# Optimization experiments

Measured on AMD Instinct MI355X. Metric: run time of the kernel, lower is better.

Reference implementation:

```python
import jax, jax.numpy as jnp
import numpy as np

NUM_HEADS = 12


def _quantize_feat(feat, embed):
    # feat: [B,H,M,d], embed: [H,K,d] -> nearest codebook vector per token
    # squared euclidean distance (same argmin as cdist p=2)
    f2 = jnp.sum(feat * feat, axis=-1, keepdims=True)            # [B,H,M,1]
    e2 = jnp.sum(embed * embed, axis=-1)[None, :, None, :]       # [1,H,1,K]
    fe = jnp.einsum('bhmd,hkd->bhmk', feat, embed)               # [B,H,M,K]
    dist = f2 - 2.0 * fe + e2
    idx = jnp.argmin(dist, axis=-1)                              # [B,H,M]
    quant = jnp.take_along_axis(embed[None], idx[..., None], axis=2)  # [B,H,M,d]
    return quant


def setup_inputs() -> dict:
    key = jax.random.key(0)
    ks = jax.random.split(key, 6)
    B, N, C, H, K = 64, 197, 768, NUM_HEADS, 50
    d = C // H
    return {
        'x': jax.random.normal(ks[0], (B, N, C), jnp.float32),
        'qkv_w': jax.random.normal(ks[1], (3 * C, C), jnp.float32) * (C ** -0.5),
        'proj_w': jax.random.normal(ks[2], (C, C), jnp.float32) * (C ** -0.5),
        'proj_b': jnp.zeros((C,), jnp.float32),
        'q_embed': jax.random.normal(ks[3], (H, K, d), jnp.float32),
        'k_embed': jax.random.normal(ks[4], (H, K, d), jnp.float32),
    }


def reference(x, qkv_w, proj_w, proj_b, q_embed, k_embed):
    B, N, C = x.shape
    H = NUM_HEADS
    d = C // H
    scale = d ** -0.5

    qkv = jnp.einsum('bnc,oc->bno', x, qkv_w).reshape(B, N, 3, H, d)
    qkv = jnp.transpose(qkv, (2, 0, 3, 1, 4))                    # [3,B,H,N,d]
    q, k, v = qkv[0], qkv[1], qkv[2]

    attn = jax.nn.softmax(jnp.einsum('bhnd,bhmd->bhnm', q, k) * scale, axis=-1)

    # quantize all tokens except cls (index 0); cls passes through detached
    q_cls = jax.lax.stop_gradient(q[:, :, 0:1, :])
    k_cls = jax.lax.stop_gradient(k[:, :, 0:1, :])
    quant_q = _quantize_feat(q[:, :, 1:, :], q_embed)
    quant_k = _quantize_feat(k[:, :, 1:, :], k_embed)

    cat_q = jnp.concatenate((q_cls, quant_q), axis=2)
    cat_k = jnp.concatenate((k_cls, quant_k), axis=2)
    quant_attn = jax.nn.softmax(
        jnp.einsum('bhnd,bhmd->bhnm', cat_q, cat_k) * scale, axis=-1)

    # losses (matching F.mse_loss mean reduction and F.kl_div semantics,
    # where input is treated as log-probabilities)
    q_tgt = jax.lax.stop_gradient(q[:, :, 1:, :])
    k_tgt = jax.lax.stop_gradient(k[:, :, 1:, :])
    quant_loss = jnp.mean((quant_q - q_tgt) ** 2) + jnp.mean((quant_k - k_tgt) ** 2)
    attn_det = jax.lax.stop_gradient(attn)
    kl = jnp.mean(attn_det * (jnp.log(attn_det) - quant_attn))
    quant_loss = quant_loss + kl

    out = jnp.einsum('bhnm,bhmd->bhnd', quant_attn, v)           # [B,H,N,d]
    out = jnp.transpose(out, (0, 2, 1, 3)).reshape(B, N, C)
    out = jnp.einsum('bnc,oc->bno', out, proj_w) + proj_b
    return (out, quant_loss)
```

## Files before the change

kernel.cpp:

```cpp
#include <hip/hip_runtime.h>
#include <math.h>

#define NB 64
#define NN 197
#define NC 768
#define NH 12
#define ND 64
#define KCB 50
#define NM (NN-1)
#define BNROWS (NB*NN)
#define SZ ((size_t)NB*NH*NN*ND)
#define WQKV ((size_t)2304*768)
#define WPRJ ((size_t)768*768)

typedef unsigned short u16;
typedef unsigned int u32;
typedef unsigned long long u64;
typedef _Float16 h2 __attribute__((ext_vector_type(2)));
typedef _Float16 f16x4 __attribute__((ext_vector_type(4)));
typedef _Float16 f16x8 __attribute__((ext_vector_type(8)));
typedef float f32x4 __attribute__((ext_vector_type(4)));

#define GLOAD16(gp, lp) __builtin_amdgcn_global_load_lds( \
    (const __attribute__((address_space(1))) void*)(gp),  \
    (__attribute__((address_space(3))) void*)(lp), 16, 0, 0)

__device__ __forceinline__ u16 f2h(float x) {
  _Float16 h = (_Float16)x;
  return *(u16*)&h;
}
__device__ __forceinline__ float h2f(u16 b) { _Float16 h = *(_Float16*)&b; return (float)h; }

#define XQ4 ((int)(SZ/4))
#define WQ4 ((int)(WQKV/4))
#define PQ4 ((int)(WPRJ/4))
#define TOTQ4 (XQ4 + WQ4 + PQ4)

__global__ __launch_bounds__(256)
void split_all(const float* __restrict__ x, const float* __restrict__ qkv_w,
               const float* __restrict__ proj_w,
               u16* __restrict__ xh, u16* __restrict__ xl,
               u16* __restrict__ wh, u16* __restrict__ wl,
               u16* __restrict__ ph)
{
  for (int i = blockIdx.x*256 + threadIdx.x; i < TOTQ4; i += gridDim.x*256) {
    const float* src; u16* hi; u16* lo; int j;
    if (i < XQ4)            { src = x;      hi = xh; lo = xl;      j = i; }
    else if (i < XQ4+WQ4)   { src = qkv_w;  hi = wh; lo = wl;      j = i - XQ4; }
    else                    { src = proj_w; hi = ph; lo = nullptr; j = i - XQ4 - WQ4; }
    float4 v = ((const float4*)src)[j];
    _Float16 h0 = (_Float16)v.x, h1 = (_Float16)v.y, h2_ = (_Float16)v.z, h3 = (_Float16)v.w;
    uint2 hv = make_uint2((u32)*(u16*)&h0 | ((u32)*(u16*)&h1 << 16),
                          (u32)*(u16*)&h2_ | ((u32)*(u16*)&h3 << 16));
    ((uint2*)hi)[j] = hv;
    if (lo) {
      _Float16 l0 = (_Float16)(v.x - (float)h0), l1 = (_Float16)(v.y - (float)h1);
      _Float16 l2 = (_Float16)(v.z - (float)h2_), l3 = (_Float16)(v.w - (float)h3);
      uint2 lv = make_uint2((u32)*(u16*)&l0 | ((u32)*(u16*)&l1 << 16),
                            (u32)*(u16*)&l2 | ((u32)*(u16*)&l3 << 16));
      ((uint2*)lo)[j] = lv;
    }
  }
}

template<int MODE>
__global__ __launch_bounds__(256)
void gemm_mfma(const u16* __restrict__ Ah, const u16* __restrict__ Al,
               const u16* __restrict__ Wh, const u16* __restrict__ Wl,
               u16* __restrict__ qh_, u16* __restrict__ ql_,
               u16* __restrict__ kh_, u16* __restrict__ kl_, u16* __restrict__ vb_,
               const float* __restrict__ bias, float* __restrict__ dout)
{
  constexpr int NPL = (MODE == 1) ? 2 : 4;
  constexpr int NBX = (MODE == 1) ? 6 : 18;
  constexpr int NWG = NBX * 99;
  constexpr int Q8 = NWG / 8, R8 = NWG % 8;
  __shared__ u16 lds[2][NPL][4096];
  const int tid = threadIdx.x;
  const int lane = tid & 63, w = tid >> 6;
  const int wm = w >> 1, wn = w & 1;
  const int wg = blockIdx.x;
  const int xcd = wg & 7, cidx = wg >> 3;
  const int work = (xcd < R8 ? xcd*(Q8+1) : R8*(Q8+1) + (xcd-R8)*Q8) + cidx;
  const int row0 = (work / NBX) * 128, col0 = (work % NBX) * 128;
  const bool dolo = (MODE == 0) && (col0 < 1536);

  f32x4 acc[4][4];
  #pragma unroll
  for (int mi = 0; mi < 4; ++mi)
    #pragma unroll
    for (int ni = 0; ni < 4; ++ni) acc[mi][ni] = (f32x4){0.f, 0.f, 0.f, 0.f};

  auto stage = [&](int buf, int kt) {
    const int c0 = kt * 32;
    #pragma unroll
    for (int j = 0; j < 2; ++j) {
      const int r0 = w*32 + j*16;
      const int lrow = r0 + (lane >> 2);
      const int slot = (lane & 3) ^ (lrow & 3);
      int ar = row0 + lrow; if (ar > BNROWS-1) ar = BNROWS-1;
      const size_t ga = (size_t)ar * 768 + c0 + slot*8;
      const size_t gb = (size_t)(col0 + lrow) * 768 + c0 + slot*8;
      GLOAD16(Ah + ga, &lds[buf][0][r0*32]);
      GLOAD16(Wh + gb, &lds[buf][1][r0*32]);
      if constexpr (MODE == 0) {
        if (dolo) {
          GLOAD16(Al + ga, &lds[buf][2][r0*32]);
          GLOAD16(Wl + gb, &lds[buf][3][r0*32]);
        }
      }
    }
  };

  auto compute = [&](int buf) {
    f16x8 ah[4], bh[4];
    const int g = lane >> 4;
    int offa[4], offb[4];
    #pragma unroll
    for (int mi = 0; mi < 4; ++mi) {
      int arow = wm*64 + mi*16 + (lane & 15);
      offa[mi] = arow*32 + ((g ^ (arow & 3)) << 3);
      ah[mi] = *(const f16x8*)&lds[buf][0][offa[mi]];
    }
    #pragma unroll
    for (int ni = 0; ni < 4; ++ni) {
      int brow = wn*64 + ni*16 + (lane & 15);
      offb[ni] = brow*32 + ((g ^ (brow & 3)) << 3);
      bh[ni] = *(const f16x8*)&lds[buf][1][offb[ni]];
    }
    #pragma unroll
    for (int mi = 0; mi < 4; ++mi)
      #pragma unroll
      for (int ni = 0; ni < 4; ++ni)
        acc[mi][ni] = __builtin_amdgcn_mfma_f32_16x16x32_f16(ah[mi], bh[ni], acc[mi][ni], 0, 0, 0);
    if constexpr (MODE == 0) {
      if (dolo) {
        f16x8 al[4], bl[4];
        #pragma unroll
        for (int mi = 0; mi < 4; ++mi) al[mi] = *(const f16x8*)&lds[buf][2][offa[mi]];
        #pragma unroll
        for (int ni = 0; ni < 4; ++ni) bl[ni] = *(const f16x8*)&lds[buf][3][offb[ni]];
        #pragma unroll
        for (int mi = 0; mi < 4; ++mi)
          #pragma unroll
          for (int ni = 0; ni < 4; ++ni) {
            acc[mi][ni] = __builtin_amdgcn_mfma_f32_16x16x32_f16(ah[mi], bl[ni], acc[mi][ni], 0, 0, 0);
            acc[mi][ni] = __builtin_amdgcn_mfma_f32_16x16x32_f16(al[mi], bh[ni], acc[mi][ni], 0, 0, 0);
          }
      }
    }
  };

  stage(0, 0);
  asm volatile("s_waitcnt vmcnt(0)" ::: "memory");
  __syncthreads();
  int cur = 0;
  for (int kt = 0; kt < 24; ++kt) {
    if (kt < 23) stage(cur ^ 1, kt + 1);
    compute(cur);
    asm volatile("s_waitcnt vmcnt(0)" ::: "memory");
    __syncthreads();
    cur ^= 1;
  }

  float* biasl = nullptr;
  if constexpr (MODE == 1) {
    biasl = (float*)&lds[0][0][0];
    if (tid < 128) biasl[tid] = bias[col0 + tid];
    __syncthreads();
  }
  #pragma unroll
  for (int mi = 0; mi < 4; ++mi) {
    #pragma unroll
    for (int t = 0; t < 4; ++t) {
      int r = row0 + wm*64 + mi*16 + (lane >> 4)*4 + t;
      if (r >= BNROWS) continue;
      if constexpr (MODE == 0) {
        int b_ = r / 197, n_ = r - b_*197;
        #pragma unroll
        for (int ni = 0; ni < 4; ++ni) {
          int o = col0 + wn*64 + ni*16 + (lane & 15);
          float val = acc[mi][ni][t];
          int tq = o / 768, rem = o - tq*768;
          int hh = rem >> 6, dd = rem & 63;
          size_t dst = ((size_t)(b_*12 + hh)*197 + n_)*64 + dd;
          u16 hi = f2h(val);
          if (tq == 0)      { qh_[dst] = hi; ql_[dst] = f2h(val - h2f(hi)); }
          else if (tq == 1) { kh_[dst] = hi; kl_[dst] = f2h(val - h2f(hi)); }
          else              vb_[dst] = hi;
        }
      } else {
        #pragma unroll
        for (int ni = 0; ni < 4; ++ni) {
          int o = col0 + wn*64 + ni*16 + (lane & 15);
          dout[(size_t)r*768 + o] = acc[mi][ni][t] + biasl[o - col0];
        }
      }
    }
  }
}

__global__ __launch_bounds__(256)
void quant_mfma(const float* __restrict__ x, const float* __restrict__ qkv_w,
                const u16* __restrict__ qh, const u16* __restrict__ ql,
                const u16* __restrict__ kh, const u16* __restrict__ kl,
                const float* __restrict__ qe, const float* __restrict__ ke,
                u16* __restrict__ cq, u16* __restrict__ ck, float* __restrict__ pq)
{
  __shared__ __align__(16) float El[KCB*66];
  __shared__ __align__(16) u16 Ehi[64*64];
  __shared__ __align__(16) u16 Elo[64*64];
  __shared__ double e2d[KCB];
  __shared__ int idxb[NM];
  __shared__ float wred[4];
  const int tid = threadIdx.x;
  const int bh = blockIdx.x;
  const int which = blockIdx.y;
  const int b_ = bh / 12, h_ = bh - b_*12;
  const u16* feath = which ? kh : qh;
  const u16* featl = which ? kl : ql;
  const float* emb  = which ? ke : qe;
  u16* dst = which ? ck : cq;
  const size_t base = (size_t)bh * (197*64);
  const int lane = tid & 63, w = tid >> 6;
  const int ln = lane & 15, g = lane >> 4;

  for (int idx = tid; idx < KCB*64; idx += 256) {
    int kk = idx >> 6, i = idx & 63;
    float v = emb[h_*(KCB*64) + idx];
    El[kk*66 + i] = v;
    _Float16 hv = (_Float16)v;
    Ehi[idx] = *(u16*)&hv;
    _Float16 lv = (_Float16)(v - (float)hv);
    Elo[idx] = *(u16*)&lv;
  }
  for (int idx = tid; idx < 14*64; idx += 256) {
    Ehi[KCB*64 + idx] = 0; Elo[KCB*64 + idx] = 0;
  }
  if (tid >= 64 && tid < 128) {
    int i = tid - 64;
    dst[base + i] = feath[base + i];
  }
  __syncthreads();
  if (tid < KCB) {
    double s = 0.0;
    for (int i = 0; i < 64; ++i) { double e = (double)El[tid*66 + i]; s += e*e; }
    e2d[tid] = s;
  }
  __syncthreads();

  f16x8 Eah[4][2], Eal[4][2];
  float e2l[4][4];
  #pragma unroll
  for (int t = 0; t < 4; ++t) {
    #pragma unroll
    for (int s = 0; s < 2; ++s) {
      int off = (t*16 + ln)*64 + s*32 + g*8;
      Eah[t][s] = *(const f16x8*)&Ehi[off];
      Eal[t][s] = *(const f16x8*)&Elo[off];
    }
    #pragma unroll
    for (int r = 0; r < 4; ++r) {
      int c = t*16 + g*4 + r;
      e2l[t][r] = (c < KCB) ? (float)e2d[c] : 1e30f;
    }
  }

  float msum = 0.f;
  for (int nt = w; nt < 13; nt += 4) {
    int tok = nt*16 + ln;
    int tokc = tok < NM ? tok : NM-1;
    const u16* fh = feath + base + (size_t)(tokc+1)*64;
    const u16* fl = featl + base + (size_t)(tokc+1)*64;
    f16x8 fqh[2], fql[2];
    float f2 = 0.f;
    #pragma unroll
    for (int s = 0; s < 2; ++s) {
      uint4 uh = *(const uint4*)(fh + s*32 + g*8);
      uint4 ul = *(const uint4*)(fl + s*32 + g*8);
      fqh[s] = *(f16x8*)&uh;
      fql[s] = *(f16x8*)&ul;
      #pragma unroll
      for (int i = 0; i < 8; ++i) {
        float q = (float)fqh[s][i] + (float)fql[s][i];
        f2 = fmaf(q, q, f2);
      }
    }
    f32x4 dacc[4];
    #pragma unroll
    for (int t = 0; t < 4; ++t) dacc[t] = (f32x4){0.f,0.f,0.f,0.f};
    #pragma unroll
    for (int t = 0; t < 4; ++t)
      #pragma unroll
      for (int s = 0; s < 2; ++s) {
        dacc[t] = __builtin_amdgcn_mfma_f32_16x16x32_f16(Eah[t][s], fqh[s], dacc[t], 0, 0, 0);
        dacc[t] = __builtin_amdgcn_mfma_f32_16x16x32_f16(Eah[t][s], fql[s], dacc[t], 0, 0, 0);
        dacc[t] = __builtin_amdgcn_mfma_f32_16x16x32_f16(Eal[t][s], fqh[s], dacc[t], 0, 0, 0);
      }
    float d1 = 1e38f, d2 = 1e38f; int idx = 0;
    #pragma unroll
    for (int t = 0; t < 4; ++t)
      #pragma unroll
      for (int r = 0; r < 4; ++r) {
        int c = t*16 + g*4 + r;
        float d = fmaf(-2.f, dacc[t][r], e2l[t][r]);
        if (d < d1) { d2 = d1; d1 = d; idx = c; }
        else if (d < d2) d2 = d;
      }
    #pragma unroll
    for (int off = 16; off <= 32; off <<= 1) {
      float od1 = __shfl_xor(d1, off), od2 = __shfl_xor(d2, off);
      int   oi  = __shfl_xor(idx, off);
      float of2 = __shfl_xor(f2, off);
      f2 += of2;
      if (od1 < d1 || (od1 == d1 && oi < idx)) {
        d2 = fminf(d1, od2); d1 = od1; idx = oi;
      } else {
        d2 = fminf(d2, od1);
      }
    }
    bool valid = tok < NM;
    bool exact = false;
    u64 flags = __ballot(g == 0 && valid && (d2 - d1) < 1e-3f);
    while (flags) {
      int src = __ffsll(flags) - 1;
      flags &= flags - 1;
      int mrow = 1 + nt*16 + src;
      const float* xrow = x + (size_t)(b_*197 + mrow)*768;
      const float* wrow = qkv_w + (size_t)(which*768 + h_*64 + lane)*768;
      double qd0 = 0.0, qd1 = 0.0, qd2 = 0.0, qd3 = 0.0;
      for (int c = 0; c < 768; c += 4) {
        qd0 = fma((double)xrow[c],   (double)wrow[c],   qd0);
        qd1 = fma((double)xrow[c+1], (double)wrow[c+1], qd1);
        qd2 = fma((double)xrow[c+2], (double)wrow[c+2], qd2);
        qd3 = fma((double)xrow[c+3], (double)wrow[c+3], qd3);
      }
      double qd = (qd0 + qd1) + (qd2 + qd3);
      double bb = 1e300; int bi = 0;
      for (int kk = 0; kk < KCB; ++kk) {
        double df = qd - (double)El[kk*66 + lane];
        double sq = df*df;
        #pragma unroll
        for (int off = 32; off > 0; off >>= 1) sq += __shfl_xor(sq, off);
        if (sq < bb) { bb = sq; bi = kk; }
      }
      if (ln == src) { idx = bi; d1 = (float)bb; exact = true; }
    }
    if (g == 0 && valid) {
      idxb[tok] = idx;
      msum += exact ? d1 : (d1 + f2);
    }
  }
  __syncthreads();

  for (int idx = tid; idx < NM*64; idx += 256) {
    int mm = idx >> 6, i = idx & 63;
    dst[base + (size_t)(mm+1)*64 + i] = f2h(El[idxb[mm]*66 + i]);
  }

  #pragma unroll
  for (int off = 8; off > 0; off >>= 1) msum += __shfl_down(msum, off);
  if (lane == 0) wred[w] = msum;
  __syncthreads();
  if (tid == 0) pq[which*768 + bh] = wred[0]+wred[1]+wred[2]+wred[3];
}

__global__ __launch_bounds__(256)
void fused_attn_mfma(const u16* __restrict__ qh, const u16* __restrict__ kh,
                     const u16* __restrict__ cq, const u16* __restrict__ ck,
                     const u16* __restrict__ vb,
                     u16* __restrict__ aoh, float* __restrict__ pkl)
{
  __shared__ __align__(16) u16 Kf[200*64];
  __shared__ __align__(16) u16 CKf[200*64];
  __shared__ __align__(16) u16 Vt[64*212];
  __shared__ float wred[4];
  const int tid = threadIdx.x;
  const int bh = blockIdx.x;
  const int b_ = bh / 12, h_ = bh - b_*12;
  const size_t base = (size_t)bh * (197*64);
  const u32* kh32 = (const u32*)kh;
  const u32* ck32 = (const u32*)ck;
  const u32* vb32 = (const u32*)vb;
  const size_t base2 = base >> 1;

  for (int idx = tid; idx < 197*32; idx += 256) {
    int m = idx >> 5, j = idx & 31;
    int dsti = m*32 + (((j >> 2) ^ (m & 7)) << 2) + (j & 3);
    ((u32*)Kf)[dsti] = kh32[base2 + idx];
    ((u32*)CKf)[dsti] = ck32[base2 + idx];
    u32 v2 = vb32[base2 + idx];
    Vt[(2*j)*212 + m]   = (u16)(v2 & 0xffff);
    Vt[(2*j+1)*212 + m] = (u16)(v2 >> 16);
  }
  for (int idx = tid; idx < 96; idx += 256) {
    int m = 197 + (idx >> 5), j = idx & 31;
    int dsti = m*32 + (((j >> 2) ^ (m & 7)) << 2) + (j & 3);
    ((u32*)Kf)[dsti] = 0; ((u32*)CKf)[dsti] = 0;
  }
  for (int idx = tid; idx < 64*15; idx += 256) {
    int d = idx / 15, mc = 197 + idx % 15;
    Vt[d*212 + mc] = 0;
  }
  __syncthreads();

  const int lane = tid & 63, w = tid >> 6;
  const int ln = lane & 15, g = lane >> 4;
  float klacc = 0.f;

  for (int nt = w; nt < 13; nt += 4) {
    const int n0 = nt*16;
    const int nb = n0 + ln;
    f16x8 fq[2], fcq[2];
    #pragma unroll
    for (int s = 0; s < 2; ++s) {
      uint4 qu = *(const uint4*)(qh + base + (size_t)nb*64 + s*32 + g*8);
      fq[s] = *(f16x8*)&qu;
      uint4 cu = *(const uint4*)(cq + base + (size_t)nb*64 + s*32 + g*8);
      fcq[s] = *(f16x8*)&cu;
    }

    float Ma = -3e38f, Mq = -3e38f;
    float aS = 0.f, aT = 0.f, qS = 0.f, cross = 0.f;
    f32x4 ov[4];
    #pragma unroll
    for (int dt = 0; dt < 4; ++dt) ov[dt] = (f32x4){0.f,0.f,0.f,0.f};

    for (int t = 0; t < 13; ++t) {
      int mrow = t*16 + ln; if (mrow > 199) mrow = 199;
      const char* kb8 = (const char*)Kf + mrow*128;
      const char* cb8 = (const char*)CKf + mrow*128;
      int sw = (mrow & 7) << 4;
      f32x4 sa = (f32x4){0.f,0.f,0.f,0.f}, sq = (f32x4){0.f,0.f,0.f,0.f};
      sa = __builtin_amdgcn_mfma_f32_16x16x32_f16(*(const f16x8*)(kb8 + (( g     <<4) ^ sw)), fq[0], sa, 0,0,0);
      sa = __builtin_amdgcn_mfma_f32_16x16x32_f16(*(const f16x8*)(kb8 + (((4+g)<<4) ^ sw)), fq[1], sa, 0,0,0);
      sq = __builtin_amdgcn_mfma_f32_16x16x32_f16(*(const f16x8*)(cb8 + (( g     <<4) ^ sw)), fcq[0], sq, 0,0,0);
      sq = __builtin_amdgcn_mfma_f32_16x16x32_f16(*(const f16x8*)(cb8 + (((4+g)<<4) ^ sw)), fcq[1], sq, 0,0,0);
      int mbase = t*16 + g*4;
      float tma = -3e38f, tmq = -3e38f;
      #pragma unroll
      for (int r = 0; r < 4; ++r) {
        bool v = (mbase + r) < 197;
        tma = fmaxf(tma, v ? sa[r] : -3e38f);
        tmq = fmaxf(tmq, v ? sq[r] : -3e38f);
      }
      tma = fmaxf(tma, __shfl_xor(tma, 16)); tma = fmaxf(tma, __shfl_xor(tma, 32));
      tmq = fmaxf(tmq, __shfl_xor(tmq, 16)); tmq = fmaxf(tmq, __shfl_xor(tmq, 32));
      float Ma2 = fmaxf(Ma, tma), Mq2 = fmaxf(Mq, tmq);
      float sca = __expf(0.125f*(Ma - Ma2));
      float scq = __expf(0.125f*(Mq - Mq2));
      Ma = Ma2; Mq = Mq2;
      aS *= sca; aT *= sca; qS *= scq; cross *= sca*scq;
      float s0 = __shfl(scq, g*4+0), s1 = __shfl(scq, g*4+1);
      float s2 = __shfl(scq, g*4+2), s3 = __shfl(scq, g*4+3);
      #pragma unroll
      for (int dt = 0; dt < 4; ++dt) {
        ov[dt][0] *= s0; ov[dt][1] *= s1; ov[dt][2] *= s2; ov[dt][3] *= s3;
      }
      const float mla = 0.125f*Ma, mlq = 0.125f*Mq;
      float eqv[4];
      #pragma unroll
      for (int r = 0; r < 4; ++r) {
        bool v = (mbase + r) < 197;
        float ea = v ? __expf(fmaf(sa[r], 0.125f, -mla)) : 0.f;
        float eq = v ? __expf(fmaf(sq[r], 0.125f, -mlq)) : 0.f;
        aS += ea;
        aT = fmaf(ea, sa[r], aT);
        qS += eq;
        cross = fmaf(ea, eq, cross);
        eqv[r] = eq;
      }
      f16x4 qaf = {(_Float16)eqv[0], (_Float16)eqv[1], (_Float16)eqv[2], (_Float16)eqv[3]};
      #pragma unroll
      for (int dt = 0; dt < 4; ++dt) {
        f16x4 bv = *(const f16x4*)(Vt + (dt*16 + ln)*212 + t*16 + g*4);
        ov[dt] = __builtin_amdgcn_mfma_f32_16x16x16f16(qaf, bv, ov[dt], 0, 0, 0);
      }
    }
    aS += __shfl_xor(aS, 16); aS += __shfl_xor(aS, 32);
    aT += __shfl_xor(aT, 16); aT += __shfl_xor(aT, 32);
    qS += __shfl_xor(qS, 16); qS += __shfl_xor(qS, 32);
    cross += __shfl_xor(cross, 16); cross += __shfl_xor(cross, 32);

    if (g == 0 && nb < 197) {
      float rowkl = 0.125f*(aT/aS) - 0.125f*Ma - __logf(aS) - cross/(aS*qS);
      klacc += rowkl;
    }
    #pragma unroll
    for (int r = 0; r < 4; ++r) {
      int nl = g*4 + r;
      int nglob = n0 + nl;
      if (nglob >= 197) continue;
      float qSn = __shfl(qS, nl);
      float inv = __frcp_rn(qSn);
      size_t obase = ((size_t)(b_*197 + nglob))*768 + h_*64;
      #pragma unroll
      for (int dt = 0; dt < 4; ++dt)
        aoh[obase + dt*16 + ln] = f2h(ov[dt][r] * inv);
    }
  }

  #pragma unroll
  for (int off = 32; off > 0; off >>= 1) klacc += __shfl_down(klacc, off);
  if (lane == 0) wred[w] = klacc;
  __syncthreads();
  if (tid == 0) pkl[bh] = wred[0] + wred[1] + wred[2] + wred[3];
}

__global__ __launch_bounds__(256)
void finalize_kernel(const float* __restrict__ pq, const float* __restrict__ pkl,
                     float* __restrict__ dout)
{
  __shared__ double red[256];
  const int tid = threadIdx.x;
  double s0 = 0.0, s1 = 0.0;
  for (int i = tid; i < 1536; i += 256) s0 += (double)pq[i];
  for (int i = tid; i < 768; i += 256) s1 += (double)pkl[i];
  red[tid] = s0; __syncthreads();
  for (int off = 128; off > 0; off >>= 1) { if (tid < off) red[tid] += red[tid+off]; __syncthreads(); }
  double mse = red[0];
  __syncthreads();
  red[tid] = s1; __syncthreads();
  for (int off = 128; off > 0; off >>= 1) { if (tid < off) red[tid] += red[tid+off]; __syncthreads(); }
  double kl = red[0];
  if (tid == 0) dout[SZ] = (float)(mse / 9633792.0 + kl / 29805312.0);
}

extern "C" void kernel_launch(void* const* d_in, const int* in_sizes, int n_in,
                              void* d_out, int out_size, void* d_ws, size_t ws_size,
                              hipStream_t stream)
{
  const float* x      = (const float*)d_in[0];
  const float* qkv_w  = (const float*)d_in[1];
  const float* proj_w = (const float*)d_in[2];
  const float* proj_b = (const float*)d_in[3];
  const float* qe     = (const float*)d_in[4];
  const float* ke     = (const float*)d_in[5];
  float* out = (float*)d_out;

  u16* ws16 = (u16*)d_ws;
  u16* qh_ = ws16;
  u16* ql_ = qh_ + SZ;
  u16* kh_ = ql_ + SZ;
  u16* kl_ = kh_ + SZ;
  u16* vb_ = kl_ + SZ;
  u16* cq_ = vb_ + SZ;
  u16* ck_ = cq_ + SZ;
  u16* aoh_= ck_ + SZ;
  u16* xh_ = aoh_ + SZ;
  u16* xl_ = xh_ + SZ;
  u16* wh_ = xl_ + SZ;
  u16* wl_ = wh_ + WQKV;
  u16* ph_ = wl_ + WQKV;
  float* pq_ = (float*)(ph_ + WPRJ);
  float* pkl_= pq_ + 1536;

  dim3 blk(256);
  split_all<<<dim3(2048), blk, 0, stream>>>(x, qkv_w, proj_w, xh_, xl_, wh_, wl_, ph_);
  gemm_mfma<0><<<dim3(99*18), blk, 0, stream>>>(xh_, xl_, wh_, wl_, qh_, ql_, kh_, kl_, vb_, nullptr, nullptr);
  quant_mfma<<<dim3(768, 2), blk, 0, stream>>>(x, qkv_w, qh_, ql_, kh_, kl_, qe, ke, cq_, ck_, pq_);
  fused_attn_mfma<<<dim3(768), blk, 0, stream>>>(qh_, kh_, cq_, ck_, vb_, aoh_, pkl_);
  gemm_mfma<1><<<dim3(99*6), blk, 0, stream>>>(aoh_, nullptr, ph_, nullptr, nullptr, nullptr, nullptr, nullptr, nullptr, proj_b, out);
  finalize_kernel<<<dim3(1), blk, 0, stream>>>(pq_, pkl_, out);
}
```

Baseline: 335.4 us.

## Stage QKV GEMM epilogue through LDS for 16-byte coalesced stores; serpentine tile order

The QKV-projection GEMM epilogue now writes each wave's 16x64 fp16 hi/lo sub-tiles into a per-wave LDS scratch area, then reads them back as 16-byte vectors and stores contiguous 128-byte rows into the head-major q/k/v layout. This replaces scattered 2-byte global stores. The head and q/k/v selection is hoisted per wave, since each wave's 64 columns map to a single head. Tile order also goes serpentine across columns on alternate row blocks, which may improve cache reuse of the shared weight and activation tiles. The change adds LDS traffic and wait instructions in the epilogue, and it reuses the pipeline LDS buffers, which relies on the main loop's final barrier.

```diff
diff --git a/kernel.cpp b/kernel.cpp
--- a/kernel.cpp
+++ b/kernel.cpp
@@ -82,7 +82,10 @@
   const int wg = blockIdx.x;
   const int xcd = wg & 7, cidx = wg >> 3;
   const int work = (xcd < R8 ? xcd*(Q8+1) : R8*(Q8+1) + (xcd-R8)*Q8) + cidx;
-  const int row0 = (work / NBX) * 128, col0 = (work % NBX) * 128;
+  const int wrow = work / NBX;
+  const int wc = work - wrow*NBX;
+  const int coli = (wrow & 1) ? (NBX-1-wc) : wc;
+  const int row0 = wrow * 128, col0 = coli * 128;
   const bool dolo = (MODE == 0) && (col0 < 1536);
 
   f32x4 acc[4][4];
@@ -163,33 +166,58 @@
     cur ^= 1;
   }
 
-  float* biasl = nullptr;
-  if constexpr (MODE == 1) {
-    biasl = (float*)&lds[0][0][0];
+  if constexpr (MODE == 0) {
+    u16* sc = ((u16*)lds) + w*2304;
+    const int ch = col0 + wn*64;
+    const int tq = ch / 768;
+    const int hh = (ch - tq*768) >> 6;
+    u16* dsth = (tq == 0) ? qh_ : (tq == 1 ? kh_ : vb_);
+    u16* dstl = (tq == 0) ? ql_ : kl_;
+    #pragma unroll
+    for (int mi = 0; mi < 4; ++mi) {
+      #pragma unroll
+      for (int ni = 0; ni < 4; ++ni) {
+        #pragma unroll
+        for (int t = 0; t < 4; ++t) {
+          int rl = (lane >> 4)*4 + t;
+          int cl = ni*16 + (lane & 15);
+          float val = acc[mi][ni][t];
+          u16 hi = f2h(val);
+          sc[rl*72 + cl] = hi;
+          if (tq < 2) sc[1152 + rl*72 + cl] = f2h(val - h2f(hi));
+        }
+      }
+      asm volatile("s_waitcnt lgkmcnt(0)" ::: "memory");
+      __builtin_amdgcn_sched_barrier(0);
+      #pragma unroll
+      for (int pass = 0; pass < 2; ++pass) {
+        int slot = pass*64 + lane;
+        int rl = slot >> 3, seg = slot & 7;
+        int r = row0 + wm*64 + mi*16 + rl;
+        if (r < BNROWS) {
+          int b_ = r / 197, n_ = r - b_*197;
+          size_t dst = ((size_t)(b_*12 + hh)*197 + n_)*64 + seg*8;
+          uint4 hv = *(const uint4*)&sc[rl*72 + seg*8];
+          *(uint4*)(dsth + dst) = hv;
+          if (tq < 2) {
+            uint4 lv = *(const uint4*)&sc[1152 + rl*72 + seg*8];
+            *(uint4*)(dstl + dst) = lv;
+          }
+        }
+      }
+      asm volatile("s_waitcnt lgkmcnt(0)" ::: "memory");
+      __builtin_amdgcn_sched_barrier(0);
+    }
+  } else {
+    float* biasl = (float*)&lds[0][0][0];
     if (tid < 128) biasl[tid] = bias[col0 + tid];
     __syncthreads();
-  }
-  #pragma unroll
-  for (int mi = 0; mi < 4; ++mi) {
-    #pragma unroll
-    for (int t = 0; t < 4; ++t) {
-      int r = row0 + wm*64 + mi*16 + (lane >> 4)*4 + t;
-      if (r >= BNROWS) continue;
-      if constexpr (MODE == 0) {
-        int b_ = r / 197, n_ = r - b_*197;
-        #pragma unroll
-        for (int ni = 0; ni < 4; ++ni) {
-          int o = col0 + wn*64 + ni*16 + (lane & 15);
-          float val = acc[mi][ni][t];
-          int tq = o / 768, rem = o - tq*768;
-          int hh = rem >> 6, dd = rem & 63;
-          size_t dst = ((size_t)(b_*12 + hh)*197 + n_)*64 + dd;
-          u16 hi = f2h(val);
-          if (tq == 0)      { qh_[dst] = hi; ql_[dst] = f2h(val - h2f(hi)); }
-          else if (tq == 1) { kh_[dst] = hi; kl_[dst] = f2h(val - h2f(hi)); }
-          else              vb_[dst] = hi;
-        }
-      } else {
+    #pragma unroll
+    for (int mi = 0; mi < 4; ++mi) {
+      #pragma unroll
+      for (int t = 0; t < 4; ++t) {
+        int r = row0 + wm*64 + mi*16 + (lane >> 4)*4 + t;
+        if (r >= BNROWS) continue;
         #pragma unroll
         for (int ni = 0; ni < 4; ++ni) {
           int o = col0 + wn*64 + ni*16 + (lane & 15);
```

After: 320.4 us. 4.4% less time.
